# Optimization experiments

Measured on AMD Instinct MI355X. Metric: run time of the kernel, lower is better.

## Reference

```python
import jax, jax.numpy as jnp
import numpy as np

NEG = -10000.0  # fp16-safe mask value, as in the torch module


def prelu(x, a):
    # nn.PReLU() default: single learnable slope shared across channels
    return jnp.where(x >= 0, x, a * x)


def setup_inputs() -> dict:
    key = jax.random.key(0)
    ks = jax.random.split(key, 9)
    B, L, D = 2048, 200, 128
    H1, H2 = 256, 128
    query = jax.random.normal(ks[0], (B, D), dtype=jnp.float32)
    keys = jax.random.normal(ks[1], (B, L, D), dtype=jnp.float32)
    mask = jax.random.randint(ks[2], (B, L), 0, 2, dtype=jnp.int32)
    s1 = 1.0 / np.sqrt(4 * D)
    s2 = 1.0 / np.sqrt(H1)
    s3 = 1.0 / np.sqrt(H2)
    W1 = jax.random.uniform(ks[3], (H1, 4 * D), minval=-s1, maxval=s1, dtype=jnp.float32)
    b1 = jax.random.uniform(ks[4], (H1,), minval=-s1, maxval=s1, dtype=jnp.float32)
    W2 = jax.random.uniform(ks[5], (H2, H1), minval=-s2, maxval=s2, dtype=jnp.float32)
    b2 = jax.random.uniform(ks[6], (H2,), minval=-s2, maxval=s2, dtype=jnp.float32)
    W3 = jax.random.uniform(ks[7], (1, H2), minval=-s3, maxval=s3, dtype=jnp.float32)
    b3 = jax.random.uniform(ks[8], (1,), minval=-s3, maxval=s3, dtype=jnp.float32)
    a1 = jnp.asarray(0.25, dtype=jnp.float32)  # PReLU init
    a2 = jnp.asarray(0.25, dtype=jnp.float32)
    return {"query": query, "keys": keys, "mask": mask,
            "W1": W1, "b1": b1, "a1": a1, "W2": W2, "b2": b2, "a2": a2,
            "W3": W3, "b3": b3}


def reference(query, keys, mask, W1, b1, a1, W2, b2, a2, W3, b3):
    B, L, D = keys.shape
    q = jnp.broadcast_to(query[:, None, :], (B, L, D))
    # [B, L, 4D] concat feature (query, key, diff, product)
    att_in = jnp.concatenate([q, keys, q - keys, q * keys], axis=-1)
    h = prelu(jnp.einsum('blf,hf->blh', att_in, W1) + b1, a1)
    h = prelu(jnp.einsum('blh,gh->blg', h, W2) + b2, a2)
    scores = (jnp.einsum('blg,og->blo', h, W3) + b3)[..., 0]  # [B, L]
    scores = jnp.where(mask == 0, NEG, scores)
    w = jax.nn.softmax(scores, axis=-1)
    w = jnp.where(mask == 0, 0.0, w)
    # weighted sum over history -> user interest [B, D]
    return jnp.einsum('bl,bld->bd', w, keys)
```

## Files before the change

### kernel.cpp

```cpp
#include <hip/hip_runtime.h>
#include <hip/hip_bf16.h>
#include <cstdint>

#define NEGV (-10000.0f)

typedef short bf16x8 __attribute__((ext_vector_type(8)));
typedef short bf16x4 __attribute__((ext_vector_type(4)));
typedef float f32x4 __attribute__((ext_vector_type(4)));

__device__ __forceinline__ short f2bf(float f) {
  union { float f; uint32_t u; } v; v.f = f;
  uint32_t u = v.u + 0x7fffu + ((v.u >> 16) & 1u);
  return (short)(u >> 16);
}
__device__ __forceinline__ float b2f(short s) {
  union { uint32_t u; float f; } v; v.u = ((uint32_t)(uint16_t)s) << 16;
  return v.f;
}
__device__ __forceinline__ uint32_t pk2(float lo, float hi) {
  union { __hip_bfloat162 h2; uint32_t u; } cv;
  cv.h2.x = __float2bfloat16(lo);
  cv.h2.y = __float2bfloat16(hi);
  return cv.u;
}

__device__ __forceinline__ void bar() {
  __builtin_amdgcn_sched_barrier(0);
  asm volatile("s_waitcnt lgkmcnt(0)" ::: "memory");
  __builtin_amdgcn_s_barrier();
  __builtin_amdgcn_sched_barrier(0);
}

__global__ void prep_weights(const float* __restrict__ W1, const float* __restrict__ W2,
                             short* __restrict__ Wk, short* __restrict__ Wd,
                             short* __restrict__ W2b) {
  int idx = blockIdx.x * 256 + threadIdx.x;
  if (idx < 32768) {
    int h = idx >> 7, d = idx & 127;
    Wk[idx] = f2bf(W1[h * 512 + 128 + d] - W1[h * 512 + 256 + d]);
  } else if (idx < 65536) {
    int i = idx - 32768;
    int h = i >> 7, d = i & 127;
    Wd[i] = f2bf(W1[h * 512 + 384 + d]);
  } else {
    int i = idx - 65536;
    W2b[i] = f2bf(W2[i]);
  }
}

__global__ void prep_u(const float* __restrict__ query, const float* __restrict__ W1,
                       const float* __restrict__ b1, float* __restrict__ U) {
  __shared__ float q8[8][128];
  int tid = threadIdx.x;
  int b0 = blockIdx.x * 8;
  for (int i = tid; i < 1024; i += 256)
    q8[i >> 7][i & 127] = query[(size_t)(b0 + (i >> 7)) * 128 + (i & 127)];
  __syncthreads();
  int h = tid;
  const float4* w0 = (const float4*)(W1 + (size_t)h * 512);
  const float4* w1 = (const float4*)(W1 + (size_t)h * 512 + 256);
  float acc[8];
  float bb = b1[h];
#pragma unroll
  for (int i = 0; i < 8; ++i) acc[i] = bb;
  for (int d4 = 0; d4 < 32; ++d4) {
    float4 wa = w0[d4], wb = w1[d4];
    float wv0 = wa.x + wb.x, wv1 = wa.y + wb.y, wv2 = wa.z + wb.z, wv3 = wa.w + wb.w;
#pragma unroll
    for (int i = 0; i < 8; ++i) {
      float4 qv = ((const float4*)q8[i])[d4];
      acc[i] += wv0 * qv.x + wv1 * qv.y + wv2 * qv.z + wv3 * qv.w;
    }
  }
#pragma unroll
  for (int i = 0; i < 8; ++i) U[(size_t)(b0 + i) * 256 + h] = acc[i];
}

__global__ __launch_bounds__(256, 2) void din_fused(
    const float* __restrict__ query, const float* __restrict__ keys,
    const int* __restrict__ mask,
    const float* __restrict__ b2p, const float* __restrict__ a1p,
    const float* __restrict__ a2p, const float* __restrict__ W3,
    const float* __restrict__ U, const short* __restrict__ Wk,
    const short* __restrict__ Wd, const short* __restrict__ W2b,
    float* __restrict__ out) {
  __shared__ short Kt[2][16 * 128];
  __shared__ short H1[2][16 * 256];
  __shared__ float wred[4][208];
  __shared__ float Ul[256];
  __shared__ float b2l[128];
  __shared__ float w3l[128];
  __shared__ float wl[208];
  __shared__ float red[8];
  __shared__ float opart[8][128];

  const int tid = threadIdx.x;
  const int b = blockIdx.x;
  const int lane = tid & 63, wid = tid >> 6;
  const int lr = lane & 15, lg = lane >> 4;

  const float a1 = a1p[0], a2 = a2p[0];

  Ul[tid] = U[(size_t)b * 256 + tid];
  if (tid < 128) { b2l[tid] = b2p[tid]; w3l[tid] = W3[tid]; }

  bf16x8 mf[4][4];
  {
    const float* qrow = query + (size_t)b * 128;
#pragma unroll
    for (int nt = 0; nt < 4; ++nt) {
      int h = wid * 64 + nt * 16 + lr;
#pragma unroll
      for (int ks = 0; ks < 4; ++ks) {
        int d0 = ks * 32 + lg * 8;
        bf16x8 wk = *(const bf16x8*)(Wk + h * 128 + d0);
        bf16x8 wd = *(const bf16x8*)(Wd + h * 128 + d0);
        float4 q0 = *(const float4*)(qrow + d0);
        float4 q1 = *(const float4*)(qrow + d0 + 4);
        float qv[8] = {q0.x, q0.y, q0.z, q0.w, q1.x, q1.y, q1.z, q1.w};
        float mv[8];
#pragma unroll
        for (int j = 0; j < 8; ++j) mv[j] = b2f(wk[j]) + b2f(wd[j]) * qv[j];
        union { bf16x8 v; uint32_t u[4]; } mm;
#pragma unroll
        for (int j = 0; j < 4; ++j) mm.u[j] = pk2(mv[2 * j], mv[2 * j + 1]);
        mf[nt][ks] = mm.v;
      }
    }
  }
  bf16x8 w2f[2][8];
#pragma unroll
  for (int nt2 = 0; nt2 < 2; ++nt2) {
    int g = wid * 32 + nt2 * 16 + lr;
#pragma unroll
    for (int ks = 0; ks < 8; ++ks)
      w2f[nt2][ks] = *(const bf16x8*)(W2b + g * 256 + ks * 32 + lg * 8);
  }

  const int srow = tid >> 4;
  const int scol = (tid & 15) * 8;
  const int ssw = (srow & 7) << 3;

  float4 h0a, h0b;
  {
    const float4* kp4 = (const float4*)(keys + ((size_t)b * 200 + srow) * 128 + scol);
    float4 s0 = kp4[0], s1 = kp4[1];
    union { bf16x8 v; uint32_t u[4]; } w;
    w.u[0] = pk2(s0.x, s0.y); w.u[1] = pk2(s0.z, s0.w);
    w.u[2] = pk2(s1.x, s1.y); w.u[3] = pk2(s1.z, s1.w);
    *(bf16x8*)(&Kt[0][srow * 128 + (scol ^ ssw)]) = w.v;
    const float4* kp4b = (const float4*)(keys + ((size_t)b * 200 + 16 + srow) * 128 + scol);
    h0a = kp4b[0]; h0b = kp4b[1];
  }
  bar();

  for (int t = 0; t < 13; ++t) {
    const int buf = t & 1;

    float4 n0, n1;
    if (t < 11) {
      int gl = (t + 2) * 16 + srow;
      n0 = n1 = make_float4(0.f, 0.f, 0.f, 0.f);
      if (gl < 200) {
        const float4* kp4 = (const float4*)(keys + ((size_t)b * 200 + gl) * 128 + scol);
        n0 = kp4[0]; n1 = kp4[1];
      }
    }

    const int sw = (lr & 7) << 3;
    bf16x8 kf[4];
#pragma unroll
    for (int ks = 0; ks < 4; ++ks)
      kf[ks] = *(const bf16x8*)(&Kt[buf][lr * 128 + ((ks * 32 + lg * 8) ^ sw)]);
    f32x4 acc[4];
#pragma unroll
    for (int nt = 0; nt < 4; ++nt)
#pragma unroll
      for (int r = 0; r < 4; ++r) acc[nt][r] = Ul[wid * 64 + nt * 16 + lg * 4 + r];
    __builtin_amdgcn_s_setprio(1);
#pragma unroll
    for (int ks = 0; ks < 4; ++ks)
#pragma unroll
      for (int nt = 0; nt < 4; ++nt)
        acc[nt] = __builtin_amdgcn_mfma_f32_16x16x32_bf16(mf[nt][ks], kf[ks], acc[nt], 0, 0, 0);
    __builtin_amdgcn_s_setprio(0);
    short* h1b = H1[buf];
#pragma unroll
    for (int nt = 0; nt < 4; ++nt) {
      float v0 = acc[nt][0], v1 = acc[nt][1], v2 = acc[nt][2], v3 = acc[nt][3];
      v0 = (v0 >= 0.f) ? v0 : a1 * v0;
      v1 = (v1 >= 0.f) ? v1 : a1 * v1;
      v2 = (v2 >= 0.f) ? v2 : a1 * v2;
      v3 = (v3 >= 0.f) ? v3 : a1 * v3;
      union { bf16x4 v; uint32_t u[2]; } hh;
      hh.u[0] = pk2(v0, v1); hh.u[1] = pk2(v2, v3);
      int h0 = wid * 64 + nt * 16 + lg * 4;
      *(bf16x4*)(&h1b[lr * 256 + (h0 ^ sw)]) = hh.v;
    }

    if (t < 12) {
      union { bf16x8 v; uint32_t u[4]; } w;
      w.u[0] = pk2(h0a.x, h0a.y); w.u[1] = pk2(h0a.z, h0a.w);
      w.u[2] = pk2(h0b.x, h0b.y); w.u[3] = pk2(h0b.z, h0b.w);
      *(bf16x8*)(&Kt[buf ^ 1][srow * 128 + (scol ^ ssw)]) = w.v;
    }
    bar();

    f32x4 acc2[2];
#pragma unroll
    for (int nt2 = 0; nt2 < 2; ++nt2)
#pragma unroll
      for (int r = 0; r < 4; ++r) acc2[nt2][r] = b2l[wid * 32 + nt2 * 16 + lg * 4 + r];
    __builtin_amdgcn_s_setprio(1);
#pragma unroll
    for (int ks = 0; ks < 8; ++ks) {
      bf16x8 hf = *(const bf16x8*)(&h1b[lr * 256 + ((ks * 32 + lg * 8) ^ sw)]);
      acc2[0] = __builtin_amdgcn_mfma_f32_16x16x32_bf16(w2f[0][ks], hf, acc2[0], 0, 0, 0);
      acc2[1] = __builtin_amdgcn_mfma_f32_16x16x32_bf16(w2f[1][ks], hf, acc2[1], 0, 0, 0);
    }
    __builtin_amdgcn_s_setprio(0);
    float s = 0.f;
#pragma unroll
    for (int nt2 = 0; nt2 < 2; ++nt2)
#pragma unroll
      for (int r = 0; r < 4; ++r) {
        float v = acc2[nt2][r];
        v = (v >= 0.f) ? v : a2 * v;
        s += v * w3l[wid * 32 + nt2 * 16 + lg * 4 + r];
      }
    s += __shfl_xor(s, 16);
    s += __shfl_xor(s, 32);
    if (lg == 0) wred[wid][t * 16 + lr] = s;

    if (t < 11) { h0a = n0; h0b = n1; }
  }
  bar();

  float val = NEGV;
  int mk = 0;
  if (tid < 200) {
    mk = mask[(size_t)b * 200 + tid];
    float sc = wred[0][tid] + wred[1][tid] + wred[2][tid] + wred[3][tid];
    val = mk ? sc : NEGV;
  }
  float m = val;
#pragma unroll
  for (int off = 1; off < 64; off <<= 1) m = fmaxf(m, __shfl_xor(m, off));
  if (lane == 0) red[wid] = m;
  bar();
  float smax = fmaxf(fmaxf(red[0], red[1]), fmaxf(red[2], red[3]));
  float pex = (tid < 200 && mk) ? __expf(val - smax) : 0.f;
  float s = pex;
#pragma unroll
  for (int off = 1; off < 64; off <<= 1) s += __shfl_xor(s, off);
  if (lane == 0) red[4 + wid] = s;
  bar();
  float ssum = red[4] + red[5] + red[6] + red[7];
  float winv = (ssum > 0.f) ? 1.f / ssum : 0.f;
  if (tid < 208) wl[tid] = (tid < 200) ? pex * winv : 0.f;
  bar();

  {
    const int d4 = (tid & 31) << 2;
    const int slice = tid >> 5;
    float ax = 0.f, ay = 0.f, az = 0.f, aw = 0.f;
    for (int l = slice; l < 200; l += 8) {
      float wv = wl[l];
      float4 kv = *(const float4*)(keys + ((size_t)b * 200 + l) * 128 + d4);
      ax += wv * kv.x; ay += wv * kv.y; az += wv * kv.z; aw += wv * kv.w;
    }
    *(float4*)(&opart[slice][d4]) = make_float4(ax, ay, az, aw);
  }
  __syncthreads();
  if (tid < 128) {
    float acc = 0.f;
#pragma unroll
    for (int i = 0; i < 8; ++i) acc += opart[i][tid];
    out[(size_t)b * 128 + tid] = acc;
  }
}

extern "C" void kernel_launch(void* const* d_in, const int* in_sizes, int n_in,
                              void* d_out, int out_size, void* d_ws, size_t ws_size,
                              hipStream_t stream) {
  const float* query = (const float*)d_in[0];
  const float* keys  = (const float*)d_in[1];
  const int*   maskp = (const int*)d_in[2];
  const float* W1    = (const float*)d_in[3];
  const float* b1    = (const float*)d_in[4];
  const float* a1    = (const float*)d_in[5];
  const float* W2    = (const float*)d_in[6];
  const float* b2    = (const float*)d_in[7];
  const float* a2    = (const float*)d_in[8];
  const float* W3    = (const float*)d_in[9];
  float* out = (float*)d_out;

  float* U   = (float*)d_ws;
  short* Wk  = (short*)((char*)d_ws + 2097152);
  short* Wd  = Wk + 32768;
  short* W2b = Wd + 32768;

  prep_weights<<<384, 256, 0, stream>>>(W1, W2, Wk, Wd, W2b);
  prep_u<<<256, 256, 0, stream>>>(query, W1, b1, U);
  din_fused<<<2048, 256, 0, stream>>>(query, keys, maskp, b2, a1, a2, W3,
                                      U, Wk, Wd, W2b, out);
}
```

Before: 153.0 us.

## Software-pipeline layer-2 MFMA one tile behind layer-1 in the key loop

Restructures the per-tile loop so layer-2 for tile t-1 runs before layer-1 for tile t, reading H1 from the opposite buffer, with an epilogue for the last tile. This lets the loop use a single barrier per iteration instead of waiting between the two layers. It depends on H1 double buffering being correct across iterations. The extra epilogue adds code size and register pressure.

```diff
diff --git a/kernel.cpp b/kernel.cpp
--- a/kernel.cpp
+++ b/kernel.cpp
@@ -154,6 +154,8 @@
   }
   bar();
 
+  const int sw = (lr & 7) << 3;
+
   for (int t = 0; t < 13; ++t) {
     const int buf = t & 1;
 
@@ -167,35 +169,65 @@
       }
     }
 
-    const int sw = (lr & 7) << 3;
-    bf16x8 kf[4];
-#pragma unroll
-    for (int ks = 0; ks < 4; ++ks)
-      kf[ks] = *(const bf16x8*)(&Kt[buf][lr * 128 + ((ks * 32 + lg * 8) ^ sw)]);
-    f32x4 acc[4];
-#pragma unroll
-    for (int nt = 0; nt < 4; ++nt)
-#pragma unroll
-      for (int r = 0; r < 4; ++r) acc[nt][r] = Ul[wid * 64 + nt * 16 + lg * 4 + r];
-    __builtin_amdgcn_s_setprio(1);
-#pragma unroll
-    for (int ks = 0; ks < 4; ++ks)
+    if (t >= 1) {
+      const short* h1p = H1[buf ^ 1];
+      f32x4 acc2[2];
+#pragma unroll
+      for (int nt2 = 0; nt2 < 2; ++nt2)
+#pragma unroll
+        for (int r = 0; r < 4; ++r) acc2[nt2][r] = b2l[wid * 32 + nt2 * 16 + lg * 4 + r];
+      __builtin_amdgcn_s_setprio(1);
+#pragma unroll
+      for (int ks = 0; ks < 8; ++ks) {
+        bf16x8 hf = *(const bf16x8*)(&h1p[lr * 256 + ((ks * 32 + lg * 8) ^ sw)]);
+        acc2[0] = __builtin_amdgcn_mfma_f32_16x16x32_bf16(w2f[0][ks], hf, acc2[0], 0, 0, 0);
+        acc2[1] = __builtin_amdgcn_mfma_f32_16x16x32_bf16(w2f[1][ks], hf, acc2[1], 0, 0, 0);
+      }
+      __builtin_amdgcn_s_setprio(0);
+      float s = 0.f;
+#pragma unroll
+      for (int nt2 = 0; nt2 < 2; ++nt2)
+#pragma unroll
+        for (int r = 0; r < 4; ++r) {
+          float v = acc2[nt2][r];
+          v = (v >= 0.f) ? v : a2 * v;
+          s += v * w3l[wid * 32 + nt2 * 16 + lg * 4 + r];
+        }
+      s += __shfl_xor(s, 16);
+      s += __shfl_xor(s, 32);
+      if (lg == 0) wred[wid][(t - 1) * 16 + lr] = s;
+    }
+
+    {
+      bf16x8 kf[4];
+#pragma unroll
+      for (int ks = 0; ks < 4; ++ks)
+        kf[ks] = *(const bf16x8*)(&Kt[buf][lr * 128 + ((ks * 32 + lg * 8) ^ sw)]);
+      f32x4 acc[4];
 #pragma unroll
       for (int nt = 0; nt < 4; ++nt)
-        acc[nt] = __builtin_amdgcn_mfma_f32_16x16x32_bf16(mf[nt][ks], kf[ks], acc[nt], 0, 0, 0);
-    __builtin_amdgcn_s_setprio(0);
-    short* h1b = H1[buf];
-#pragma unroll
-    for (int nt = 0; nt < 4; ++nt) {
-      float v0 = acc[nt][0], v1 = acc[nt][1], v2 = acc[nt][2], v3 = acc[nt][3];
-      v0 = (v0 >= 0.f) ? v0 : a1 * v0;
-      v1 = (v1 >= 0.f) ? v1 : a1 * v1;
-      v2 = (v2 >= 0.f) ? v2 : a1 * v2;
-      v3 = (v3 >= 0.f) ? v3 : a1 * v3;
-      union { bf16x4 v; uint32_t u[2]; } hh;
-      hh.u[0] = pk2(v0, v1); hh.u[1] = pk2(v2, v3);
-      int h0 = wid * 64 + nt * 16 + lg * 4;
-      *(bf16x4*)(&h1b[lr * 256 + (h0 ^ sw)]) = hh.v;
+#pragma unroll
+        for (int r = 0; r < 4; ++r) acc[nt][r] = Ul[wid * 64 + nt * 16 + lg * 4 + r];
+      __builtin_amdgcn_s_setprio(1);
+#pragma unroll
+      for (int ks = 0; ks < 4; ++ks)
+#pragma unroll
+        for (int nt = 0; nt < 4; ++nt)
+          acc[nt] = __builtin_amdgcn_mfma_f32_16x16x32_bf16(mf[nt][ks], kf[ks], acc[nt], 0, 0, 0);
+      __builtin_amdgcn_s_setprio(0);
+      short* h1b = H1[buf];
+#pragma unroll
+      for (int nt = 0; nt < 4; ++nt) {
+        float v0 = acc[nt][0], v1 = acc[nt][1], v2 = acc[nt][2], v3 = acc[nt][3];
+        v0 = (v0 >= 0.f) ? v0 : a1 * v0;
+        v1 = (v1 >= 0.f) ? v1 : a1 * v1;
+        v2 = (v2 >= 0.f) ? v2 : a1 * v2;
+        v3 = (v3 >= 0.f) ? v3 : a1 * v3;
+        union { bf16x4 v; uint32_t u[2]; } hh;
+        hh.u[0] = pk2(v0, v1); hh.u[1] = pk2(v2, v3);
+        int h0 = wid * 64 + nt * 16 + lg * 4;
+        *(bf16x4*)(&h1b[lr * 256 + (h0 ^ sw)]) = hh.v;
+      }
     }
 
     if (t < 12) {
@@ -204,21 +236,24 @@
       w.u[2] = pk2(h0b.x, h0b.y); w.u[3] = pk2(h0b.z, h0b.w);
       *(bf16x8*)(&Kt[buf ^ 1][srow * 128 + (scol ^ ssw)]) = w.v;
     }
+    if (t < 11) { h0a = n0; h0b = n1; }
+
     bar();
-
+  }
+
+  {
+    const short* h1p = H1[0];
     f32x4 acc2[2];
 #pragma unroll
     for (int nt2 = 0; nt2 < 2; ++nt2)
 #pragma unroll
       for (int r = 0; r < 4; ++r) acc2[nt2][r] = b2l[wid * 32 + nt2 * 16 + lg * 4 + r];
-    __builtin_amdgcn_s_setprio(1);
 #pragma unroll
     for (int ks = 0; ks < 8; ++ks) {
-      bf16x8 hf = *(const bf16x8*)(&h1b[lr * 256 + ((ks * 32 + lg * 8) ^ sw)]);
+      bf16x8 hf = *(const bf16x8*)(&h1p[lr * 256 + ((ks * 32 + lg * 8) ^ sw)]);
       acc2[0] = __builtin_amdgcn_mfma_f32_16x16x32_bf16(w2f[0][ks], hf, acc2[0], 0, 0, 0);
       acc2[1] = __builtin_amdgcn_mfma_f32_16x16x32_bf16(w2f[1][ks], hf, acc2[1], 0, 0, 0);
     }
-    __builtin_amdgcn_s_setprio(0);
     float s = 0.f;
 #pragma unroll
     for (int nt2 = 0; nt2 < 2; ++nt2)
@@ -230,9 +265,7 @@
       }
     s += __shfl_xor(s, 16);
     s += __shfl_xor(s, 32);
-    if (lg == 0) wred[wid][t * 16 + lr] = s;
-
-    if (t < 11) { h0a = n0; h0b = n1; }
+    if (lg == 0) wred[wid][12 * 16 + lr] = s;
   }
   bar();
 
```

New measurement: 147.9 us. 3.4% less time.

## Stage all keys in LDS as bf16 and widen block to 1024 threads

Applied to the files above, without the earlier changes.

Restructures the fused DIN kernel to use 16 waves per block: each wave owns one 16-column slice of layer 1 and half of a layer-2 tile. The MLP loop becomes a software pipeline with layer 2 of the previous 32-row chunk overlapping layer 1 of the current one. All 200 key rows are kept in LDS as bf16, so the final weighted sum reads LDS instead of re-reading fp32 keys from global memory. This halves global key traffic but loses precision in the output weighted sum and raises LDS pressure, which may limit residency.

```diff
diff --git a/kernel.cpp b/kernel.cpp
--- a/kernel.cpp
+++ b/kernel.cpp
@@ -76,7 +76,7 @@
   for (int i = 0; i < 8; ++i) U[(size_t)(b0 + i) * 256 + h] = acc[i];
 }
 
-__global__ __launch_bounds__(256, 2) void din_fused(
+__global__ __launch_bounds__(1024) void din_fused(
     const float* __restrict__ query, const float* __restrict__ keys,
     const int* __restrict__ mask,
     const float* __restrict__ b2p, const float* __restrict__ a1p,
@@ -84,155 +84,161 @@
     const float* __restrict__ U, const short* __restrict__ Wk,
     const short* __restrict__ Wd, const short* __restrict__ W2b,
     float* __restrict__ out) {
-  __shared__ short Kt[2][16 * 128];
-  __shared__ short H1[2][16 * 256];
-  __shared__ float wred[4][208];
+  __shared__ short Kall[224 * 128];
+  __shared__ union {
+    short H1[2][32 * 256];
+    float opart[64][128];
+  } uH;
+  __shared__ float wred[8][224];
+  __shared__ float wl[224];
   __shared__ float Ul[256];
-  __shared__ float b2l[128];
-  __shared__ float w3l[128];
-  __shared__ float wl[208];
-  __shared__ float red[8];
-  __shared__ float opart[8][128];
+  __shared__ float red[32];
 
   const int tid = threadIdx.x;
   const int b = blockIdx.x;
   const int lane = tid & 63, wid = tid >> 6;
   const int lr = lane & 15, lg = lane >> 4;
+  const int gt = wid >> 1, lh = wid & 1;
+  const int sw = (lr & 7) << 3;
 
   const float a1 = a1p[0], a2 = a2p[0];
 
-  Ul[tid] = U[(size_t)b * 256 + tid];
-  if (tid < 128) { b2l[tid] = b2p[tid]; w3l[tid] = W3[tid]; }
-
-  bf16x8 mf[4][4];
+  if (tid < 256) Ul[tid] = U[(size_t)b * 256 + tid];
+
+  bf16x8 mf[4];
   {
     const float* qrow = query + (size_t)b * 128;
-#pragma unroll
-    for (int nt = 0; nt < 4; ++nt) {
-      int h = wid * 64 + nt * 16 + lr;
-#pragma unroll
-      for (int ks = 0; ks < 4; ++ks) {
-        int d0 = ks * 32 + lg * 8;
-        bf16x8 wk = *(const bf16x8*)(Wk + h * 128 + d0);
-        bf16x8 wd = *(const bf16x8*)(Wd + h * 128 + d0);
-        float4 q0 = *(const float4*)(qrow + d0);
-        float4 q1 = *(const float4*)(qrow + d0 + 4);
-        float qv[8] = {q0.x, q0.y, q0.z, q0.w, q1.x, q1.y, q1.z, q1.w};
-        float mv[8];
-#pragma unroll
-        for (int j = 0; j < 8; ++j) mv[j] = b2f(wk[j]) + b2f(wd[j]) * qv[j];
-        union { bf16x8 v; uint32_t u[4]; } mm;
-#pragma unroll
-        for (int j = 0; j < 4; ++j) mm.u[j] = pk2(mv[2 * j], mv[2 * j + 1]);
-        mf[nt][ks] = mm.v;
+    int h = wid * 16 + lr;
+#pragma unroll
+    for (int ks = 0; ks < 4; ++ks) {
+      int d0 = ks * 32 + lg * 8;
+      bf16x8 wk = *(const bf16x8*)(Wk + h * 128 + d0);
+      bf16x8 wd = *(const bf16x8*)(Wd + h * 128 + d0);
+      float4 q0 = *(const float4*)(qrow + d0);
+      float4 q1 = *(const float4*)(qrow + d0 + 4);
+      float qv[8] = {q0.x, q0.y, q0.z, q0.w, q1.x, q1.y, q1.z, q1.w};
+      float mv[8];
+#pragma unroll
+      for (int j = 0; j < 8; ++j) mv[j] = b2f(wk[j]) + b2f(wd[j]) * qv[j];
+      union { bf16x8 v; uint32_t u[4]; } mm;
+#pragma unroll
+      for (int j = 0; j < 4; ++j) mm.u[j] = pk2(mv[2 * j], mv[2 * j + 1]);
+      mf[ks] = mm.v;
+    }
+  }
+  bf16x8 w2f[8];
+  {
+    int g = gt * 16 + lr;
+#pragma unroll
+    for (int ks = 0; ks < 8; ++ks)
+      w2f[ks] = *(const bf16x8*)(W2b + g * 256 + ks * 32 + lg * 8);
+  }
+  float uv[4], b2v[4], w3v[4];
+#pragma unroll
+  for (int r = 0; r < 4; ++r) {
+    uv[r] = U[(size_t)b * 256 + wid * 16 + lg * 4 + r];
+    int gg = gt * 16 + lg * 4 + r;
+    b2v[r] = b2p[gg];
+    w3v[r] = W3[gg];
+  }
+
+  const int srow = tid >> 5;
+  const int sc4 = (tid & 31) * 4;
+  const int ssw = (srow & 7) << 3;
+
+  float4 rg;
+  {
+#pragma unroll
+    for (int t = 0; t < 2; ++t) {
+      int grow = t * 32 + srow;
+      float4 x = *(const float4*)(keys + ((size_t)b * 200 + grow) * 128 + sc4);
+      union { bf16x4 v; uint32_t u[2]; } w;
+      w.u[0] = pk2(x.x, x.y); w.u[1] = pk2(x.z, x.w);
+      *(bf16x4*)(&Kall[grow * 128 + (sc4 ^ ssw)]) = w.v;
+    }
+    rg = *(const float4*)(keys + ((size_t)b * 200 + 64 + srow) * 128 + sc4);
+  }
+  bar();
+
+  for (int p = 0; p < 8; ++p) {
+    const int buf = p & 1;
+
+    float4 nrg;
+    if (p <= 3) {
+      int grow = (p + 3) * 32 + srow;
+      nrg = make_float4(0.f, 0.f, 0.f, 0.f);
+      if (grow < 200)
+        nrg = *(const float4*)(keys + ((size_t)b * 200 + grow) * 128 + sc4);
+    }
+
+    if (p >= 1) {
+      const short* hr = &uH.H1[buf ^ 1][(lh * 16 + lr) * 256];
+      f32x4 acc2;
+#pragma unroll
+      for (int r = 0; r < 4; ++r) acc2[r] = b2v[r];
+      __builtin_amdgcn_s_setprio(1);
+#pragma unroll
+      for (int ks = 0; ks < 8; ++ks) {
+        bf16x8 hf = *(const bf16x8*)(&hr[(ks * 32 + lg * 8) ^ sw]);
+        acc2 = __builtin_amdgcn_mfma_f32_16x16x32_bf16(w2f[ks], hf, acc2, 0, 0, 0);
       }
-    }
-  }
-  bf16x8 w2f[2][8];
-#pragma unroll
-  for (int nt2 = 0; nt2 < 2; ++nt2) {
-    int g = wid * 32 + nt2 * 16 + lr;
-#pragma unroll
-    for (int ks = 0; ks < 8; ++ks)
-      w2f[nt2][ks] = *(const bf16x8*)(W2b + g * 256 + ks * 32 + lg * 8);
-  }
-
-  const int srow = tid >> 4;
-  const int scol = (tid & 15) * 8;
-  const int ssw = (srow & 7) << 3;
-
-  float4 h0a, h0b;
-  {
-    const float4* kp4 = (const float4*)(keys + ((size_t)b * 200 + srow) * 128 + scol);
-    float4 s0 = kp4[0], s1 = kp4[1];
-    union { bf16x8 v; uint32_t u[4]; } w;
-    w.u[0] = pk2(s0.x, s0.y); w.u[1] = pk2(s0.z, s0.w);
-    w.u[2] = pk2(s1.x, s1.y); w.u[3] = pk2(s1.z, s1.w);
-    *(bf16x8*)(&Kt[0][srow * 128 + (scol ^ ssw)]) = w.v;
-    const float4* kp4b = (const float4*)(keys + ((size_t)b * 200 + 16 + srow) * 128 + scol);
-    h0a = kp4b[0]; h0b = kp4b[1];
-  }
-  bar();
-
-  for (int t = 0; t < 13; ++t) {
-    const int buf = t & 1;
-
-    float4 n0, n1;
-    if (t < 11) {
-      int gl = (t + 2) * 16 + srow;
-      n0 = n1 = make_float4(0.f, 0.f, 0.f, 0.f);
-      if (gl < 200) {
-        const float4* kp4 = (const float4*)(keys + ((size_t)b * 200 + gl) * 128 + scol);
-        n0 = kp4[0]; n1 = kp4[1];
+      __builtin_amdgcn_s_setprio(0);
+      float s = 0.f;
+#pragma unroll
+      for (int r = 0; r < 4; ++r) {
+        float v = acc2[r];
+        v = (v >= 0.f) ? v : a2 * v;
+        s += v * w3v[r];
       }
-    }
-
-    const int sw = (lr & 7) << 3;
-    bf16x8 kf[4];
-#pragma unroll
-    for (int ks = 0; ks < 4; ++ks)
-      kf[ks] = *(const bf16x8*)(&Kt[buf][lr * 128 + ((ks * 32 + lg * 8) ^ sw)]);
-    f32x4 acc[4];
-#pragma unroll
-    for (int nt = 0; nt < 4; ++nt)
-#pragma unroll
-      for (int r = 0; r < 4; ++r) acc[nt][r] = Ul[wid * 64 + nt * 16 + lg * 4 + r];
-    __builtin_amdgcn_s_setprio(1);
-#pragma unroll
-    for (int ks = 0; ks < 4; ++ks)
-#pragma unroll
-      for (int nt = 0; nt < 4; ++nt)
-        acc[nt] = __builtin_amdgcn_mfma_f32_16x16x32_bf16(mf[nt][ks], kf[ks], acc[nt], 0, 0, 0);
-    __builtin_amdgcn_s_setprio(0);
-    short* h1b = H1[buf];
-#pragma unroll
-    for (int nt = 0; nt < 4; ++nt) {
-      float v0 = acc[nt][0], v1 = acc[nt][1], v2 = acc[nt][2], v3 = acc[nt][3];
-      v0 = (v0 >= 0.f) ? v0 : a1 * v0;
-      v1 = (v1 >= 0.f) ? v1 : a1 * v1;
-      v2 = (v2 >= 0.f) ? v2 : a1 * v2;
-      v3 = (v3 >= 0.f) ? v3 : a1 * v3;
-      union { bf16x4 v; uint32_t u[2]; } hh;
-      hh.u[0] = pk2(v0, v1); hh.u[1] = pk2(v2, v3);
-      int h0 = wid * 64 + nt * 16 + lg * 4;
-      *(bf16x4*)(&h1b[lr * 256 + (h0 ^ sw)]) = hh.v;
-    }
-
-    if (t < 12) {
-      union { bf16x8 v; uint32_t u[4]; } w;
-      w.u[0] = pk2(h0a.x, h0a.y); w.u[1] = pk2(h0a.z, h0a.w);
-      w.u[2] = pk2(h0b.x, h0b.y); w.u[3] = pk2(h0b.z, h0b.w);
-      *(bf16x8*)(&Kt[buf ^ 1][srow * 128 + (scol ^ ssw)]) = w.v;
-    }
+      s += __shfl_xor(s, 16);
+      s += __shfl_xor(s, 32);
+      if (lg == 0) wred[gt][(p - 1) * 32 + lh * 16 + lr] = s;
+    }
+
+    if (p < 7) {
+      short* h1b = uH.H1[buf];
+#pragma unroll
+      for (int s2 = 0; s2 < 2; ++s2) {
+        const int lrow = p * 32 + s2 * 16 + lr;
+        bf16x8 kf[4];
+#pragma unroll
+        for (int ks = 0; ks < 4; ++ks)
+          kf[ks] = *(const bf16x8*)(&Kall[lrow * 128 + ((ks * 32 + lg * 8) ^ sw)]);
+        f32x4 acc;
+#pragma unroll
+        for (int r = 0; r < 4; ++r) acc[r] = uv[r];
+        __builtin_amdgcn_s_setprio(1);
+#pragma unroll
+        for (int ks = 0; ks < 4; ++ks)
+          acc = __builtin_amdgcn_mfma_f32_16x16x32_bf16(mf[ks], kf[ks], acc, 0, 0, 0);
+        __builtin_amdgcn_s_setprio(0);
+        float v0 = acc[0], v1 = acc[1], v2 = acc[2], v3 = acc[3];
+        v0 = (v0 >= 0.f) ? v0 : a1 * v0;
+        v1 = (v1 >= 0.f) ? v1 : a1 * v1;
+        v2 = (v2 >= 0.f) ? v2 : a1 * v2;
+        v3 = (v3 >= 0.f) ? v3 : a1 * v3;
+        union { bf16x4 v; uint32_t u[2]; } hh;
+        hh.u[0] = pk2(v0, v1); hh.u[1] = pk2(v2, v3);
+        *(bf16x4*)(&h1b[(s2 * 16 + lr) * 256 + ((wid * 16 + lg * 4) ^ sw)]) = hh.v;
+      }
+    }
+
+    if (p <= 4) {
+      int grow = (p + 2) * 32 + srow;
+      union { bf16x4 v; uint32_t u[2]; } w;
+      w.u[0] = pk2(rg.x, rg.y); w.u[1] = pk2(rg.z, rg.w);
+      *(bf16x4*)(&Kall[grow * 128 + (sc4 ^ ssw)]) = w.v;
+    }
+    if (p <= 3) rg = nrg;
+
     bar();
-
-    f32x4 acc2[2];
-#pragma unroll
-    for (int nt2 = 0; nt2 < 2; ++nt2)
-#pragma unroll
-      for (int r = 0; r < 4; ++r) acc2[nt2][r] = b2l[wid * 32 + nt2 * 16 + lg * 4 + r];
-    __builtin_amdgcn_s_setprio(1);
-#pragma unroll
-    for (int ks = 0; ks < 8; ++ks) {
-      bf16x8 hf = *(const bf16x8*)(&h1b[lr * 256 + ((ks * 32 + lg * 8) ^ sw)]);
-      acc2[0] = __builtin_amdgcn_mfma_f32_16x16x32_bf16(w2f[0][ks], hf, acc2[0], 0, 0, 0);
-      acc2[1] = __builtin_amdgcn_mfma_f32_16x16x32_bf16(w2f[1][ks], hf, acc2[1], 0, 0, 0);
-    }
-    __builtin_amdgcn_s_setprio(0);
+  }
+
+  if (tid < 224) {
     float s = 0.f;
 #pragma unroll
-    for (int nt2 = 0; nt2 < 2; ++nt2)
-#pragma unroll
-      for (int r = 0; r < 4; ++r) {
-        float v = acc2[nt2][r];
-        v = (v >= 0.f) ? v : a2 * v;
-        s += v * w3l[wid * 32 + nt2 * 16 + lg * 4 + r];
-      }
-    s += __shfl_xor(s, 16);
-    s += __shfl_xor(s, 32);
-    if (lg == 0) wred[wid][t * 16 + lr] = s;
-
-    if (t < 11) { h0a = n0; h0b = n1; }
+    for (int w = 0; w < 8; ++w) s += wred[w][tid];
+    wl[tid] = s;
   }
   bar();
 
@@ -240,42 +246,50 @@
   int mk = 0;
   if (tid < 200) {
     mk = mask[(size_t)b * 200 + tid];
-    float sc = wred[0][tid] + wred[1][tid] + wred[2][tid] + wred[3][tid];
-    val = mk ? sc : NEGV;
+    val = mk ? wl[tid] : NEGV;
   }
   float m = val;
 #pragma unroll
   for (int off = 1; off < 64; off <<= 1) m = fmaxf(m, __shfl_xor(m, off));
   if (lane == 0) red[wid] = m;
   bar();
-  float smax = fmaxf(fmaxf(red[0], red[1]), fmaxf(red[2], red[3]));
+  float smax = red[0];
+#pragma unroll
+  for (int i = 1; i < 16; ++i) smax = fmaxf(smax, red[i]);
   float pex = (tid < 200 && mk) ? __expf(val - smax) : 0.f;
   float s = pex;
 #pragma unroll
   for (int off = 1; off < 64; off <<= 1) s += __shfl_xor(s, off);
-  if (lane == 0) red[4 + wid] = s;
-  bar();
-  float ssum = red[4] + red[5] + red[6] + red[7];
+  if (lane == 0) red[16 + wid] = s;
+  bar();
+  float ssum = 0.f;
+#pragma unroll
+  for (int i = 0; i < 16; ++i) ssum += red[16 + i];
   float winv = (ssum > 0.f) ? 1.f / ssum : 0.f;
-  if (tid < 208) wl[tid] = (tid < 200) ? pex * winv : 0.f;
+  if (tid < 224) wl[tid] = (tid < 200) ? pex * winv : 0.f;
   bar();
 
   {
-    const int d4 = (tid & 31) << 2;
-    const int slice = tid >> 5;
-    float ax = 0.f, ay = 0.f, az = 0.f, aw = 0.f;
-    for (int l = slice; l < 200; l += 8) {
+    const int d0 = (tid & 15) * 8;
+    const int slice = tid >> 4;
+    float a[8];
+#pragma unroll
+    for (int j = 0; j < 8; ++j) a[j] = 0.f;
+    for (int l = slice; l < 200; l += 64) {
       float wv = wl[l];
-      float4 kv = *(const float4*)(keys + ((size_t)b * 200 + l) * 128 + d4);
-      ax += wv * kv.x; ay += wv * kv.y; az += wv * kv.z; aw += wv * kv.w;
-    }
-    *(float4*)(&opart[slice][d4]) = make_float4(ax, ay, az, aw);
-  }
-  __syncthreads();
+      bf16x8 kv = *(const bf16x8*)(&Kall[l * 128 + (d0 ^ ((l & 7) << 3))]);
+#pragma unroll
+      for (int j = 0; j < 8; ++j) a[j] += wv * b2f(kv[j]);
+    }
+    bar();
+    *(float4*)(&uH.opart[slice][d0]) = make_float4(a[0], a[1], a[2], a[3]);
+    *(float4*)(&uH.opart[slice][d0 + 4]) = make_float4(a[4], a[5], a[6], a[7]);
+  }
+  bar();
   if (tid < 128) {
     float acc = 0.f;
 #pragma unroll
-    for (int i = 0; i < 8; ++i) acc += opart[i][tid];
+    for (int i = 0; i < 64; ++i) acc += uH.opart[i][tid];
     out[(size_t)b * 128 + tid] = acc;
   }
 }
@@ -302,6 +316,6 @@
 
   prep_weights<<<384, 256, 0, stream>>>(W1, W2, Wk, Wd, W2b);
   prep_u<<<256, 256, 0, stream>>>(query, W1, b1, U);
-  din_fused<<<2048, 256, 0, stream>>>(query, keys, maskp, b2, a1, a2, W3,
-                                      U, Wk, Wd, W2b, out);
-}
+  din_fused<<<2048, 1024, 0, stream>>>(query, keys, maskp, b2, a1, a2, W3,
+                                       U, Wk, Wd, W2b, out);
+}
```

After: 193.4 us. +26.4%, slower.
